# Optimization experiments

Measured on AMD Instinct MI355X. Metric: run time of the kernel, lower is better.

## Reference

```python
import math
import jax, jax.numpy as jnp
import numpy as np

E = 1024
H = 16
D = E // H  # 64

def _l2norm(t, eps=1e-12):
    n = jnp.sqrt(jnp.sum(t * t, axis=-1, keepdims=True))
    return t / jnp.maximum(n, eps)

def setup_inputs() -> dict:
    key = jax.random.key(0)
    ks = jax.random.split(key, 10)
    s = 0.02
    x = jax.random.normal(ks[0], (2, 4096, E), dtype=jnp.float32)
    Wq = jax.random.normal(ks[1], (E, E), dtype=jnp.float32) * s
    Wk = jax.random.normal(ks[2], (E, E), dtype=jnp.float32) * s
    Wv = jax.random.normal(ks[3], (E, E), dtype=jnp.float32) * s
    Walpha = jax.random.normal(ks[4], (E, H), dtype=jnp.float32) * s
    Wbeta = jax.random.normal(ks[5], (E, H), dtype=jnp.float32) * s
    A_log = jnp.linspace(0.0, math.log(16.0), H).astype(jnp.float32)
    dt_bias = jnp.zeros((H,), dtype=jnp.float32)
    Wgate = jax.random.normal(ks[6], (E, E), dtype=jnp.float32) * s
    Wout = jax.random.normal(ks[7], (E, E), dtype=jnp.float32) * s
    rms_w = jnp.ones((D,), dtype=jnp.float32)
    return {"x": x, "Wq": Wq, "Wk": Wk, "Wv": Wv, "Walpha": Walpha,
            "Wbeta": Wbeta, "A_log": A_log, "dt_bias": dt_bias,
            "Wgate": Wgate, "Wout": Wout, "rms_w": rms_w}

def reference(x, Wq, Wk, Wv, Walpha, Wbeta, A_log, dt_bias, Wgate, Wout, rms_w):
    b, s, _ = x.shape
    q = (x @ Wq).reshape(b, s, H, D)
    k = (x @ Wk).reshape(b, s, H, D)
    v = (x @ Wv).reshape(b, s, H, D)
    q = _l2norm(q) / math.sqrt(D)
    k = _l2norm(k)
    # gates: alpha in (0,1], beta in (0,1)   [b,s,H]
    dt = jax.nn.softplus(x @ Walpha + dt_bias)
    alpha = jnp.exp(-jnp.exp(A_log) * dt)
    beta = jax.nn.sigmoid(x @ Wbeta)

    # time-major for scan: [s,b,H,D] / [s,b,H]
    qT = jnp.moveaxis(q, 1, 0)
    kT = jnp.moveaxis(k, 1, 0)
    vT = jnp.moveaxis(v, 1, 0)
    aT = jnp.moveaxis(alpha, 1, 0)
    bT = jnp.moveaxis(beta, 1, 0)

    state0 = jnp.zeros((b, H, D, D), dtype=x.dtype)

    def step(state, inp):
        q_t, k_t, v_t, a_t, b_t = inp  # [b,H,D] x3, [b,H] x2
        state = a_t[..., None, None] * state
        stored = jnp.einsum('bhij,bhj->bhi', state, k_t)
        delta = b_t[..., None] * (v_t - stored)
        state = state + jnp.einsum('bhi,bhj->bhij', delta, k_t)
        o_t = jnp.einsum('bhij,bhj->bhi', state, q_t)
        return state, o_t

    # q,k,v are [s,b,H,D] -> per-step [b,H,D]
    qs = jnp.swapaxes(qT, 1, 2).swapaxes(1, 1)  # keep [s,b,H,D]
    _, outs = jax.lax.scan(step, state0, (qT, kT, vT, aT, bT))
    out = jnp.moveaxis(outs, 0, 1)  # [b,s,H,D]

    # RMSNorm over head_dim
    var = jnp.mean(out * out, axis=-1, keepdims=True)
    out = out * jax.lax.rsqrt(var + 1e-6) * rms_w

    out = out.reshape(b, s, E)
    gate = jax.nn.silu(x @ Wgate)
    return (out * gate) @ Wout
```

## Files before the change

kernel.cpp:

```cpp
#include <hip/hip_runtime.h>
#include <cstdint>
#include <cstddef>

typedef __bf16 bf16;
typedef __bf16 bf16x4 __attribute__((ext_vector_type(4)));
typedef __bf16 bf16x8 __attribute__((ext_vector_type(8)));
typedef float  f32x4  __attribute__((ext_vector_type(4)));

#define GLD_LDS16(gp, lp) \
  __builtin_amdgcn_global_load_lds((__attribute__((address_space(1))) void*)(gp), \
                                   (__attribute__((address_space(3))) void*)(lp), 16, 0, 0)

__device__ __forceinline__ f32x4 f32x4_zero(){ f32x4 v; v[0]=0.f; v[1]=0.f; v[2]=0.f; v[3]=0.f; return v; }

__device__ __forceinline__ f32x4 mfma16x16x32(bf16x8 a, bf16x8 b, f32x4 c){
  return __builtin_amdgcn_mfma_f32_16x16x32_bf16(a, b, c, 0, 0, 0);
}
__device__ __forceinline__ bf16x8 frag64(const bf16* base, int row0, int kk, int lane){
  return *(const bf16x8*)&base[(row0 + (lane&15))*64 + kk*32 + (lane>>4)*8];
}
__device__ __forceinline__ bf16x8 fragSwz(const bf16* base, int row0, int kk, int lane){
  const int row = row0 + (lane&15);
  const int off = (kk*32 + (lane>>4)*8) ^ ((row&7)<<3);
  return *(const bf16x8*)&base[row*64 + off];
}
struct bf2 { bf16 h, l; };
__device__ __forceinline__ bf2 split2(float v){
  bf2 r; r.h = (bf16)v; r.l = (bf16)(v - (float)r.h); return r;
}

__global__ __launch_bounds__(256) void k_cvt_x(const float* __restrict__ x,
                                               bf16* __restrict__ xh, bf16* __restrict__ xl, int n4){
  int i = blockIdx.x*256 + threadIdx.x;
  if (i < n4){
    float4 v = ((const float4*)x)[i];
    bf16x4 h, l;
    bf2 t0 = split2(v.x); h[0]=t0.h; l[0]=t0.l;
    bf2 t1 = split2(v.y); h[1]=t1.h; l[1]=t1.l;
    bf2 t2 = split2(v.z); h[2]=t2.h; l[2]=t2.l;
    bf2 t3 = split2(v.w); h[3]=t3.h; l[3]=t3.l;
    ((bf16x4*)xh)[i] = h;
    ((bf16x4*)xl)[i] = l;
  }
}

__global__ __launch_bounds__(256) void k_transpose_w(const float* __restrict__ W,
                                                     bf16* __restrict__ Wth, bf16* __restrict__ Wtl){
  __shared__ float tile[32][33];
  const int k0 = blockIdx.x*32, n0 = blockIdx.y*32;
  const int r = threadIdx.x >> 3, c4 = (threadIdx.x & 7)*4;
  float4 v = *(const float4*)&W[(size_t)(k0+r)*1024 + n0 + c4];
  tile[r][c4+0]=v.x; tile[r][c4+1]=v.y; tile[r][c4+2]=v.z; tile[r][c4+3]=v.w;
  __syncthreads();
  bf16x4 h, l;
  bf2 t0 = split2(tile[c4+0][r]); h[0]=t0.h; l[0]=t0.l;
  bf2 t1 = split2(tile[c4+1][r]); h[1]=t1.h; l[1]=t1.l;
  bf2 t2 = split2(tile[c4+2][r]); h[2]=t2.h; l[2]=t2.l;
  bf2 t3 = split2(tile[c4+3][r]); h[3]=t3.h; l[3]=t3.l;
  *(bf16x4*)&Wth[(size_t)(n0+r)*1024 + k0 + c4] = h;
  *(bf16x4*)&Wtl[(size_t)(n0+r)*1024 + k0 + c4] = l;
}

__global__ __launch_bounds__(256) void k_transpose_ab(const float* __restrict__ Wa, const float* __restrict__ Wb,
                                                      bf16* __restrict__ WabTh, bf16* __restrict__ WabTl){
  int p = blockIdx.x*256 + threadIdx.x;
  if (p < 32768){
    int o = p >> 10, k = p & 1023;
    float v = (o < 16) ? Wa[k*16 + o] : Wb[k*16 + (o-16)];
    bf2 s = split2(v);
    WabTh[p] = s.h;
    WabTl[p] = s.l;
  }
}

__global__ __launch_bounds__(256) void k_gemm3(const bf16* __restrict__ Ah, const bf16* __restrict__ Al,
                                               const bf16* __restrict__ Bth, const bf16* __restrict__ Btl,
                                               bf16* __restrict__ Cb, float* __restrict__ Cf){
  __shared__ bf16 Ash[128*32], Asl[128*32];
  __shared__ bf16 Bsh[128*32], Bsl[128*32];
  const int tid = threadIdx.x, lane = tid & 63, w = tid >> 6;
  const int wm = w >> 1, wn = w & 1;
  const size_t m0 = (size_t)blockIdx.x * 128;
  const size_t n0 = (size_t)blockIdx.y * 128;
  f32x4 acc[4][4];
  #pragma unroll
  for (int i=0;i<4;++i)
    #pragma unroll
    for (int j=0;j<4;++j) acc[i][j] = f32x4_zero();

  for (int k0 = 0; k0 < 1024; k0 += 32){
    __syncthreads();
    #pragma unroll
    for (int j = 0; j < 2; ++j){
      const int rbase = 32*w + 16*j;
      const int r = rbase + (lane >> 2);
      const int kk = k0 + (lane & 3)*8;
      GLD_LDS16(&Ah [(m0 + r)*1024 + kk], &Ash[rbase*32]);
      GLD_LDS16(&Al [(m0 + r)*1024 + kk], &Asl[rbase*32]);
      GLD_LDS16(&Bth[(n0 + r)*1024 + kk], &Bsh[rbase*32]);
      GLD_LDS16(&Btl[(n0 + r)*1024 + kk], &Bsl[rbase*32]);
    }
    __syncthreads();
    bf16x8 ah[4], al[4], bh[4], bl[4];
    #pragma unroll
    for (int t=0;t<4;++t){
      ah[t] = *(const bf16x8*)&Ash[(64*wm + 16*t + (lane&15))*32 + (lane>>4)*8];
      al[t] = *(const bf16x8*)&Asl[(64*wm + 16*t + (lane&15))*32 + (lane>>4)*8];
      bh[t] = *(const bf16x8*)&Bsh[(64*wn + 16*t + (lane&15))*32 + (lane>>4)*8];
      bl[t] = *(const bf16x8*)&Bsl[(64*wn + 16*t + (lane&15))*32 + (lane>>4)*8];
    }
    #pragma unroll
    for (int i=0;i<4;++i)
      #pragma unroll
      for (int j=0;j<4;++j){
        f32x4 t = acc[i][j];
        t = mfma16x16x32(ah[i], bh[j], t);
        t = mfma16x16x32(ah[i], bl[j], t);
        t = mfma16x16x32(al[i], bh[j], t);
        acc[i][j] = t;
      }
  }
  #pragma unroll
  for (int i=0;i<4;++i)
    #pragma unroll
    for (int j=0;j<4;++j)
      #pragma unroll
      for (int r=0;r<4;++r){
        size_t row = m0 + 64*wm + 16*i + (lane>>4)*4 + r;
        size_t col = n0 + 64*wn + 16*j + (lane&15);
        float v = acc[i][j][r];
        if (Cf) Cf[row*1024 + col] = v;
        else    Cb[row*1024 + col] = (bf16)v;
      }
}

template<int NRM>
__global__ __launch_bounds__(256) void k_gemm1(const bf16* __restrict__ Ah, const bf16* __restrict__ Bth,
                                               bf16* __restrict__ Cb, float* __restrict__ Cf){
  __shared__ bf16 Ash[128*32];
  __shared__ bf16 Bsh[128*32];
  const int tid = threadIdx.x, lane = tid & 63, w = tid >> 6;
  const int wm = w >> 1, wn = w & 1;
  const size_t m0 = (size_t)blockIdx.x * 128;
  const size_t n0 = (size_t)blockIdx.y * 128;
  f32x4 acc[4][4];
  #pragma unroll
  for (int i=0;i<4;++i)
    #pragma unroll
    for (int j=0;j<4;++j) acc[i][j] = f32x4_zero();

  for (int k0 = 0; k0 < 1024; k0 += 32){
    __syncthreads();
    #pragma unroll
    for (int j = 0; j < 2; ++j){
      const int rbase = 32*w + 16*j;
      const int r = rbase + (lane >> 2);
      const int kk = k0 + (lane & 3)*8;
      GLD_LDS16(&Ah [(m0 + r)*1024 + kk], &Ash[rbase*32]);
      GLD_LDS16(&Bth[(n0 + r)*1024 + kk], &Bsh[rbase*32]);
    }
    __syncthreads();
    bf16x8 ah[4], bh[4];
    #pragma unroll
    for (int t=0;t<4;++t){
      ah[t] = *(const bf16x8*)&Ash[(64*wm + 16*t + (lane&15))*32 + (lane>>4)*8];
      bh[t] = *(const bf16x8*)&Bsh[(64*wn + 16*t + (lane&15))*32 + (lane>>4)*8];
    }
    #pragma unroll
    for (int i=0;i<4;++i)
      #pragma unroll
      for (int j=0;j<4;++j)
        acc[i][j] = mfma16x16x32(ah[i], bh[j], acc[i][j]);
  }
  #pragma unroll
  for (int i=0;i<4;++i)
    #pragma unroll
    for (int r=0;r<4;++r){
      float sc = 1.f;
      if (NRM){
        float ss = 0.f;
        #pragma unroll
        for (int j=0;j<4;++j) ss += acc[i][j][r]*acc[i][j][r];
        ss += __shfl_xor(ss, 1); ss += __shfl_xor(ss, 2);
        ss += __shfl_xor(ss, 4); ss += __shfl_xor(ss, 8);
        sc = (NRM==1 ? 0.125f : 1.0f) / fmaxf(sqrtf(ss), 1e-12f);
      }
      #pragma unroll
      for (int j=0;j<4;++j){
        size_t row = m0 + 64*wm + 16*i + (lane>>4)*4 + r;
        size_t col = n0 + 64*wn + 16*j + (lane&15);
        float v = acc[i][j][r]*sc;
        if (Cf) Cf[row*1024 + col] = v;
        else    Cb[row*1024 + col] = (bf16)v;
      }
    }
}

__global__ __launch_bounds__(256) void k_ab_gemm(const bf16* __restrict__ xh, const bf16* __restrict__ xl,
    const bf16* __restrict__ WabTh, const bf16* __restrict__ WabTl,
    const float* __restrict__ A_log, const float* __restrict__ dt_bias,
    float* __restrict__ logA, float* __restrict__ betap){
  __shared__ bf16 Ash[2][2048], Asl[2][2048];
  const int tid = threadIdx.x, lane = tid & 63, w = tid >> 6;
  const int mt = w >> 1, nt = w & 1;
  const size_t m0 = (size_t)blockIdx.x * 32;
  const int srow = tid >> 3;
  const int scol = 8*((tid & 7) ^ (srow & 7));
  const size_t sg = (m0 + srow)*1024 + scol;

  f32x4 acc = f32x4_zero();
  GLD_LDS16(&xh[sg], &Ash[0][w*512]);
  GLD_LDS16(&xl[sg], &Asl[0][w*512]);
  for (int s = 0; s < 16; ++s){
    const int cur = s & 1;
    __syncthreads();
    if (s + 1 < 16){
      const size_t g = sg + (size_t)(s+1)*64;
      GLD_LDS16(&xh[g], &Ash[cur^1][w*512]);
      GLD_LDS16(&xl[g], &Asl[cur^1][w*512]);
    }
    const int k0 = s*64;
    #pragma unroll
    for (int kk = 0; kk < 2; ++kk){
      bf16x8 aH = fragSwz(Ash[cur], 16*mt, kk, lane);
      bf16x8 aL = fragSwz(Asl[cur], 16*mt, kk, lane);
      const size_t bo = (size_t)(16*nt + (lane&15))*1024 + k0 + kk*32 + (lane>>4)*8;
      bf16x8 bH = *(const bf16x8*)&WabTh[bo];
      bf16x8 bL = *(const bf16x8*)&WabTl[bo];
      acc = mfma16x16x32(aH, bH, acc);
      acc = mfma16x16x32(aH, bL, acc);
      acc = mfma16x16x32(aL, bH, acc);
    }
  }
  const int col = lane & 15;
  #pragma unroll
  for (int r = 0; r < 4; ++r){
    const size_t row = m0 + 16*mt + (lane>>4)*4 + r;
    float v = acc[r];
    if (nt == 0){
      float z = v + dt_bias[col];
      float dt = (z > 20.f) ? z : log1pf(expf(z));
      logA[row*16 + col] = -expf(A_log[col]) * dt;
    } else {
      betap[row*16 + col] = 1.f/(1.f + expf(-v));
    }
  }
}

__device__ __forceinline__ void load_split_tile(const float* f32, const bf16* b16,
                                                size_t tokbase, int h,
                                                bf16* Lh, bf16* Ll, int tid, int nthr){
  for (int i = tid; i < 1024; i += nthr){
    int t = i >> 4, c4 = (i & 15)*4;
    const size_t g = (tokbase + t)*1024 + (size_t)h*64 + c4;
    float4 v;
    if (f32) v = *(const float4*)&f32[g];
    else { bf16x4 b = *(const bf16x4*)&b16[g]; v.x=(float)b[0]; v.y=(float)b[1]; v.z=(float)b[2]; v.w=(float)b[3]; }
    bf16x4 hh, ll;
    bf2 s0 = split2(v.x); hh[0]=s0.h; ll[0]=s0.l;
    bf2 s1 = split2(v.y); hh[1]=s1.h; ll[1]=s1.l;
    bf2 s2 = split2(v.z); hh[2]=s2.h; ll[2]=s2.l;
    bf2 s3 = split2(v.w); hh[3]=s3.h; ll[3]=s3.l;
    const int off = c4 ^ ((t&7)<<3);
    *(bf16x4*)&Lh[t*64 + off] = hh;
    *(bf16x4*)&Ll[t*64 + off] = ll;
  }
}

__global__ __launch_bounds__(128, 4) void k_phaseA(const float* __restrict__ kf32, const bf16* __restrict__ kb16,
    const float* __restrict__ vf, const float* __restrict__ logA, const float* __restrict__ betap,
    bf16* __restrict__ Wg, bf16* __restrict__ Dg, float* __restrict__ Pg, bf16* __restrict__ Bg){
  __shared__ bf16  Kh[4096], Kl_[4096];
  __shared__ float Ef[4096];
  bf16* DT  = Kh;
  bf16* WT  = Kl_;
  bf16* KtT = (bf16*)&Ef[2048];
  const int tid = threadIdx.x, lane = tid & 63, wid = tid >> 6;
  const int c = blockIdx.x, h = blockIdx.y, b = blockIdx.z;
  const size_t tokbase = (size_t)b*4096 + (size_t)c*64;
  const size_t cbase = ((size_t)((b*16 + h)*64 + c)) * 4096;

  load_split_tile(kf32, kb16, tokbase, h, Kh, Kl_, tid, 128);
  const float bet = betap[(tokbase + lane)*16 + h];
  if (tid < 64){
    float la = logA[(tokbase + tid)*16 + h];
    #pragma unroll
    for (int dlt = 1; dlt < 64; dlt <<= 1){
      float o = __shfl_up(la, dlt);
      if (lane >= dlt) la += o;
    }
    Ef[tid] = la;
  }
  __syncthreads();

  #pragma unroll
  for (int tt = 0; tt < 2; ++tt){
    const int t0 = 32*wid + 16*tt;
    #pragma unroll
    for (int tu = 0; tu < 4; ++tu){
      f32x4 accm = f32x4_zero();
      #pragma unroll
      for (int kk = 0; kk < 2; ++kk){
        bf16x8 aH = fragSwz(Kh,  t0,    kk, lane);
        bf16x8 aL = fragSwz(Kl_, t0,    kk, lane);
        bf16x8 bH = fragSwz(Kh,  16*tu, kk, lane);
        bf16x8 bL = fragSwz(Kl_, 16*tu, kk, lane);
        accm = mfma16x16x32(aH, bH, accm);
        accm = mfma16x16x32(aH, bL, accm);
        accm = mfma16x16x32(aL, bH, accm);
      }
      #pragma unroll
      for (int r = 0; r < 4; ++r){
        int row = t0 + (lane>>4)*4 + r, col = 16*tu + (lane&15);
        float ev = (col < row) ? accm[r]*__expf(Ef[row] - Ef[col]) : 0.f;
        if (row > 0) Ef[row*64 + col] = ev;
      }
    }
  }
  __syncthreads();

  float d[64];
  {
    if (wid == 0){
      #pragma unroll
      for (int t = 0; t < 64; ++t)
        d[t] = vf[(tokbase + t)*1024 + h*64 + lane];
    } else {
      #pragma unroll
      for (int t = 0; t < 64; ++t){
        int ks = lane ^ ((t&7)<<3);
        d[t] = __expf(Ef[t]) * ((float)Kh[t*64 + ks] + (float)Kl_[t*64 + ks]);
      }
    }
    #pragma unroll
    for (int bi = 0; bi < 4; ++bi){
      #pragma unroll
      for (int tt = 0; tt < 16; ++tt){
        const int t = 16*bi + tt;
        float s = 0.f;
        #pragma unroll
        for (int j = 0; j < 16; ++j)
          if (j < tt) s += Ef[t*64 + 16*bi + j] * d[16*bi + j];
        d[t] = __shfl(bet, t) * (d[t] - s);
      }
      #pragma unroll
      for (int b2 = bi + 1; b2 < 4; ++b2)
        #pragma unroll
        for (int tt = 0; tt < 16; ++tt){
          const int t = 16*b2 + tt;
          float a0=0.f,a1=0.f,a2=0.f,a3=0.f;
          #pragma unroll
          for (int q = 0; q < 4; ++q){
            float4 e = *(const float4*)&Ef[t*64 + 16*bi + q*4];
            a0 += e.x * d[16*bi + q*4 + 0];
            a1 += e.y * d[16*bi + q*4 + 1];
            a2 += e.z * d[16*bi + q*4 + 2];
            a3 += e.w * d[16*bi + q*4 + 3];
          }
          d[t] -= (a0+a1)+(a2+a3);
        }
    }
  }
  __syncthreads();

  {
    const float gsc = __expf(Ef[63] - Ef[lane]);
    for (int i = tid; i < 4096; i += 128){
      int t = lane, j = i >> 6;
      int ks = j ^ ((t&7)<<3);
      float kv = (float)Kh[t*64 + ks] + (float)Kl_[t*64 + ks];
      KtT[j*64 + (t ^ ((j&7)<<3))] = (bf16)(gsc * kv);
    }
  }
  __syncthreads();

  const float gL = __expf(Ef[63]);
  {
    bf16* myT = wid ? WT : DT;
    #pragma unroll
    for (int s4 = 0; s4 < 16; ++s4){
      bf16x4 v4;
      v4[0]=(bf16)d[s4*4+0]; v4[1]=(bf16)d[s4*4+1];
      v4[2]=(bf16)d[s4*4+2]; v4[3]=(bf16)d[s4*4+3];
      *(bf16x4*)&myT[lane*64 + ((s4*4) ^ ((lane&7)<<3))] = v4;
    }
    bf16* myG = wid ? Wg : Dg;
    #pragma unroll
    for (int t = 0; t < 64; ++t)
      myG[cbase + (size_t)t*64 + lane] = (bf16)d[t];
  }
  __syncthreads();

  if (wid == 0){
    #pragma unroll
    for (int tj = 0; tj < 4; ++tj)
      #pragma unroll
      for (int ti = 0; ti < 4; ++ti){
        f32x4 acc = f32x4_zero();
        #pragma unroll
        for (int kk = 0; kk < 2; ++kk)
          acc = mfma16x16x32(fragSwz(KtT, 16*tj, kk, lane), fragSwz(WT, 16*ti, kk, lane), acc);
        #pragma unroll
        for (int r = 0; r < 4; ++r){
          int row = 16*tj + (lane>>4)*4 + r, col = 16*ti + (lane&15);
          Pg[cbase + (size_t)row*64 + col] = ((row == col) ? gL : 0.f) - acc[r];
        }
      }
  } else {
    #pragma unroll
    for (int ti = 0; ti < 4; ++ti)
      #pragma unroll
      for (int tj = 0; tj < 4; ++tj){
        f32x4 acc = f32x4_zero();
        #pragma unroll
        for (int kk = 0; kk < 2; ++kk)
          acc = mfma16x16x32(fragSwz(DT, 16*ti, kk, lane), fragSwz(KtT, 16*tj, kk, lane), acc);
        #pragma unroll
        for (int r = 0; r < 4; ++r){
          int row = 16*ti + (lane>>4)*4 + r, col = 16*tj + (lane&15);
          Bg[cbase + (size_t)row*64 + col] = (bf16)acc[r];
        }
      }
  }
}

__global__ __launch_bounds__(256) void k_phaseB1(const float* __restrict__ Pg, const bf16* __restrict__ Bg,
                                                 float* __restrict__ PsegT, float* __restrict__ BsegF){
  __shared__ bf16 PaccH[4096], PaccL[4096], BaccH[4096], BaccL[4096];
  __shared__ bf16 PcH[4096], PcL[4096];
  __shared__ bf16 BcS[4096];
  const int tid = threadIdx.x, lane = tid & 63, w = tid >> 6;
  const int seg = blockIdx.x;
  const size_t chain = blockIdx.y;
  f32x4 Pr[4], Br[4];
  #pragma unroll
  for (int it = 0; it < 4; ++it){
    #pragma unroll
    for (int r = 0; r < 4; ++r){
      int row = 16*w + (lane>>4)*4 + r, col = 16*it + (lane&15);
      Pr[it][r] = (row == col) ? 1.f : 0.f;
      Br[it][r] = 0.f;
    }
  }
  for (int i = 0; i < 8; ++i){
    const size_t cb = (chain*64 + (size_t)seg*8 + i)*4096;
    #pragma unroll
    for (int it = 0; it < 4; ++it)
      #pragma unroll
      for (int r = 0; r < 4; ++r){
        int row = 16*w + (lane>>4)*4 + r, col = 16*it + (lane&15);
        bf2 sp = split2(Pr[it][r]); PaccH[row*64+col] = sp.h; PaccL[row*64+col] = sp.l;
        bf2 sb = split2(Br[it][r]); BaccH[row*64+col] = sb.h; BaccL[row*64+col] = sb.l;
      }
    __syncthreads();
    for (int j = tid; j < 1024; j += 256){
      float4 pv = ((const float4*)(Pg + cb))[j];
      bf16x4 ph, pl;
      bf2 u0 = split2(pv.x); ph[0]=u0.h; pl[0]=u0.l;
      bf2 u1 = split2(pv.y); ph[1]=u1.h; pl[1]=u1.l;
      bf2 u2 = split2(pv.z); ph[2]=u2.h; pl[2]=u2.l;
      bf2 u3 = split2(pv.w); ph[3]=u3.h; pl[3]=u3.l;
      ((bf16x4*)PcH)[j] = ph; ((bf16x4*)PcL)[j] = pl;
    }
    for (int j = tid; j < 512; j += 256)
      ((uint4*)BcS)[j] = ((const uint4*)(Bg + cb))[j];
    __syncthreads();
    f32x4 nP[4], nB[4];
    #pragma unroll
    for (int it = 0; it < 4; ++it){ nP[it] = f32x4_zero(); nB[it] = f32x4_zero(); }
    #pragma unroll
    for (int kk = 0; kk < 2; ++kk){
      bf16x8 aPH = frag64(PaccH, 16*w, kk, lane), aPL = frag64(PaccL, 16*w, kk, lane);
      bf16x8 aBH = frag64(BaccH, 16*w, kk, lane), aBL = frag64(BaccL, 16*w, kk, lane);
      #pragma unroll
      for (int it = 0; it < 4; ++it){
        bf16x8 bH = frag64(PcH, 16*it, kk, lane), bL = frag64(PcL, 16*it, kk, lane);
        nP[it] = mfma16x16x32(aPH, bH, nP[it]);
        nP[it] = mfma16x16x32(aPH, bL, nP[it]);
        nP[it] = mfma16x16x32(aPL, bH, nP[it]);
        nB[it] = mfma16x16x32(aBH, bH, nB[it]);
        nB[it] = mfma16x16x32(aBH, bL, nB[it]);
        nB[it] = mfma16x16x32(aBL, bH, nB[it]);
      }
    }
    #pragma unroll
    for (int it = 0; it < 4; ++it)
      #pragma unroll
      for (int r = 0; r < 4; ++r){
        int row = 16*w + (lane>>4)*4 + r, col = 16*it + (lane&15);
        Pr[it][r] = nP[it][r];
        Br[it][r] = nB[it][r] + (float)BcS[row*64 + col];
      }
  }
  const size_t sb = (chain*8 + seg)*4096;
  #pragma unroll
  for (int it = 0; it < 4; ++it)
    #pragma unroll
    for (int r = 0; r < 4; ++r){
      int row = 16*w + (lane>>4)*4 + r, col = 16*it + (lane&15);
      PsegT[sb + (size_t)col*64 + row] = Pr[it][r];
      BsegF[sb + (size_t)row*64 + col] = Br[it][r];
    }
}

__global__ __launch_bounds__(256) void k_phaseB2(const float* __restrict__ PsegT, const float* __restrict__ BsegF,
                                                 float* __restrict__ S0g){
  __shared__ bf16 Sh[4096], Sl[4096], Ph[4096], Pl[4096];
  __shared__ float Bf[4096];
  const int tid = threadIdx.x, lane = tid & 63, w = tid >> 6;
  const size_t bid = blockIdx.x;
  f32x4 Sr[4];
  #pragma unroll
  for (int it = 0; it < 4; ++it) Sr[it] = f32x4_zero();
  for (int seg = 0; seg < 8; ++seg){
    const size_t sb  = (bid*8 + seg)*4096;
    const size_t s0b = (bid*64 + (size_t)seg*8)*4096;
    #pragma unroll
    for (int it = 0; it < 4; ++it)
      #pragma unroll
      for (int r = 0; r < 4; ++r){
        int row = 16*w + (lane>>4)*4 + r, col = 16*it + (lane&15);
        S0g[s0b + (size_t)row*64 + col] = Sr[it][r];
        bf2 sp = split2(Sr[it][r]); Sh[row*64+col] = sp.h; Sl[row*64+col] = sp.l;
      }
    __syncthreads();
    for (int j = tid; j < 1024; j += 256){
      float4 pv = ((const float4*)(PsegT + sb))[j];
      bf16x4 ph, pl;
      bf2 u0 = split2(pv.x); ph[0]=u0.h; pl[0]=u0.l;
      bf2 u1 = split2(pv.y); ph[1]=u1.h; pl[1]=u1.l;
      bf2 u2 = split2(pv.z); ph[2]=u2.h; pl[2]=u2.l;
      bf2 u3 = split2(pv.w); ph[3]=u3.h; pl[3]=u3.l;
      ((bf16x4*)Ph)[j] = ph; ((bf16x4*)Pl)[j] = pl;
      ((float4*)Bf)[j] = ((const float4*)(BsegF + sb))[j];
    }
    __syncthreads();
    f32x4 nS[4];
    #pragma unroll
    for (int it = 0; it < 4; ++it) nS[it] = f32x4_zero();
    #pragma unroll
    for (int kk = 0; kk < 2; ++kk){
      bf16x8 aH = frag64(Sh, 16*w, kk, lane), aL = frag64(Sl, 16*w, kk, lane);
      #pragma unroll
      for (int it = 0; it < 4; ++it){
        bf16x8 bH = frag64(Ph, 16*it, kk, lane), bL = frag64(Pl, 16*it, kk, lane);
        nS[it] = mfma16x16x32(aH, bH, nS[it]);
        nS[it] = mfma16x16x32(aH, bL, nS[it]);
        nS[it] = mfma16x16x32(aL, bH, nS[it]);
      }
    }
    #pragma unroll
    for (int it = 0; it < 4; ++it)
      #pragma unroll
      for (int r = 0; r < 4; ++r){
        int row = 16*w + (lane>>4)*4 + r, col = 16*it + (lane&15);
        Sr[it][r] = nS[it][r] + Bf[row*64 + col];
      }
  }
}

__global__ __launch_bounds__(256) void k_phaseB3(const float* __restrict__ Pg, const bf16* __restrict__ Bg,
                                                 float* __restrict__ S0g){
  __shared__ bf16 Sh[4096], Sl[4096], Ph[4096], Pl[4096];
  __shared__ bf16 BcS[4096];
  const int tid = threadIdx.x, lane = tid & 63, w = tid >> 6;
  const int seg = blockIdx.x;
  const size_t chain = blockIdx.y;
  const size_t segbase = chain*64 + (size_t)seg*8;
  f32x4 Sr[4];
  #pragma unroll
  for (int it = 0; it < 4; ++it)
    #pragma unroll
    for (int r = 0; r < 4; ++r){
      int row = 16*w + (lane>>4)*4 + r, col = 16*it + (lane&15);
      Sr[it][r] = S0g[segbase*4096 + (size_t)row*64 + col];
    }
  for (int i = 0; i < 7; ++i){
    const size_t cb = (segbase + i)*4096;
    #pragma unroll
    for (int it = 0; it < 4; ++it)
      #pragma unroll
      for (int r = 0; r < 4; ++r){
        int row = 16*w + (lane>>4)*4 + r, col = 16*it + (lane&15);
        bf2 sp = split2(Sr[it][r]); Sh[row*64+col] = sp.h; Sl[row*64+col] = sp.l;
      }
    __syncthreads();
    for (int j = tid; j < 1024; j += 256){
      float4 pv = ((const float4*)(Pg + cb))[j];
      bf16x4 ph, pl;
      bf2 u0 = split2(pv.x); ph[0]=u0.h; pl[0]=u0.l;
      bf2 u1 = split2(pv.y); ph[1]=u1.h; pl[1]=u1.l;
      bf2 u2 = split2(pv.z); ph[2]=u2.h; pl[2]=u2.l;
      bf2 u3 = split2(pv.w); ph[3]=u3.h; pl[3]=u3.l;
      ((bf16x4*)Ph)[j] = ph; ((bf16x4*)Pl)[j] = pl;
    }
    for (int j = tid; j < 512; j += 256)
      ((uint4*)BcS)[j] = ((const uint4*)(Bg + cb))[j];
    __syncthreads();
    f32x4 nS[4];
    #pragma unroll
    for (int it = 0; it < 4; ++it) nS[it] = f32x4_zero();
    #pragma unroll
    for (int kk = 0; kk < 2; ++kk){
      bf16x8 aH = frag64(Sh, 16*w, kk, lane), aL = frag64(Sl, 16*w, kk, lane);
      #pragma unroll
      for (int it = 0; it < 4; ++it){
        bf16x8 bH = frag64(Ph, 16*it, kk, lane), bL = frag64(Pl, 16*it, kk, lane);
        nS[it] = mfma16x16x32(aH, bH, nS[it]);
        nS[it] = mfma16x16x32(aH, bL, nS[it]);
        nS[it] = mfma16x16x32(aL, bH, nS[it]);
      }
    }
    const size_t outb = (segbase + i + 1)*4096;
    #pragma unroll
    for (int it = 0; it < 4; ++it)
      #pragma unroll
      for (int r = 0; r < 4; ++r){
        int row = 16*w + (lane>>4)*4 + r, col = 16*it + (lane&15);
        float v = nS[it][r] + (float)BcS[row*64 + col];
        Sr[it][r] = v;
        S0g[outb + (size_t)row*64 + col] = v;
      }
  }
}

__global__ __launch_bounds__(256, 2) void k_phaseC(
    const float* __restrict__ qf32, const bf16* __restrict__ qb16,
    const float* __restrict__ kf32, const bf16* __restrict__ kb16,
    const bf16* __restrict__ gf, const float* __restrict__ logA,
    const float* __restrict__ S0g, const bf16* __restrict__ Wg, const bf16* __restrict__ Dg,
    const float* __restrict__ rms_w, bf16* __restrict__ yh, bf16* __restrict__ yl){
  __shared__ bf16 Qh[4096], Ql[4096], Kh[4096], Klo[4096];
  __shared__ bf16 Wl_[4096], Dl_[4096];
  __shared__ bf16 S0h[4096], S0l[4096];
  __shared__ bf16 AAg[4096];
  __shared__ bf16 BDt[4096];
  const int tid = threadIdx.x, lane = tid & 63, w = tid >> 6;
  const int c = blockIdx.x, h = blockIdx.y, b = blockIdx.z;
  const size_t tokbase = (size_t)b*4096 + (size_t)c*64;
  const size_t cbase = ((size_t)((b*16 + h)*64 + c)) * 4096;

  load_split_tile(qf32, qb16, tokbase, h, Qh, Ql, tid, 256);
  load_split_tile(kf32, kb16, tokbase, h, Kh, Klo, tid, 256);
  for (int i = tid; i < 512; i += 256){
    int r = i >> 3, d = r*8 + ((i&7) ^ (r&7));
    ((uint4*)Wl_)[d] = ((const uint4*)(Wg + cbase))[i];
    ((uint4*)Dl_)[d] = ((const uint4*)(Dg + cbase))[i];
  }
  for (int i = tid; i < 1024; i += 256){
    float4 v = ((const float4*)(S0g + cbase))[i];
    bf16x4 sh, sl;
    bf2 t0 = split2(v.x); sh[0]=t0.h; sl[0]=t0.l;
    bf2 t1 = split2(v.y); sh[1]=t1.h; sl[1]=t1.l;
    bf2 t2 = split2(v.z); sh[2]=t2.h; sl[2]=t2.l;
    bf2 t3 = split2(v.w); sh[3]=t3.h; sl[3]=t3.l;
    int t = i >> 4, off = ((i&15)*4) ^ ((t&7)<<3);
    *(bf16x4*)&S0h[t*64 + off] = sh;
    *(bf16x4*)&S0l[t*64 + off] = sl;
  }
  float la = logA[(tokbase + lane)*16 + h];
  #pragma unroll
  for (int dlt = 1; dlt < 64; dlt <<= 1){
    float o = __shfl_up(la, dlt);
    if (lane >= dlt) la += o;
  }
  __syncthreads();

  {
    const int t0 = 16*w;
    #pragma unroll
    for (int tu = 0; tu < 4; ++tu){
      f32x4 accm = f32x4_zero();
      #pragma unroll
      for (int kk = 0; kk < 2; ++kk){
        bf16x8 aH = fragSwz(Qh,  t0,    kk, lane);
        bf16x8 aL = fragSwz(Ql,  t0,    kk, lane);
        bf16x8 bH = fragSwz(Kh,  16*tu, kk, lane);
        bf16x8 bL = fragSwz(Klo, 16*tu, kk, lane);
        accm = mfma16x16x32(aH, bH, accm);
        accm = mfma16x16x32(aH, bL, accm);
        accm = mfma16x16x32(aL, bH, accm);
      }
      #pragma unroll
      for (int r = 0; r < 4; ++r){
        int row = t0 + (lane>>4)*4 + r, col = 16*tu + (lane&15);
        float lgr = __shfl(la, row), lgc = __shfl(la, col);
        float v = (col <= row) ? accm[r]*__expf(lgr - lgc) : 0.f;
        AAg[row*64 + (col ^ ((row&7)<<3))] = (bf16)v;
      }
    }
  }
  {
    const int i0 = 16*w;
    #pragma unroll
    for (int tu = 0; tu < 4; ++tu){
      f32x4 accm = f32x4_zero();
      #pragma unroll
      for (int kk = 0; kk < 2; ++kk){
        bf16x8 aH = fragSwz(S0h, i0,    kk, lane);
        bf16x8 aL = fragSwz(S0l, i0,    kk, lane);
        bf16x8 bb = fragSwz(Wl_, 16*tu, kk, lane);
        accm = mfma16x16x32(aH, bb, accm);
        accm = mfma16x16x32(aL, bb, accm);
      }
      #pragma unroll
      for (int r = 0; r < 4; ++r){
        int row = i0 + (lane>>4)*4 + r, col = 16*tu + (lane&15);
        float v = (float)Dl_[col*64 + (row ^ ((col&7)<<3))] - accm[r];
        BDt[row*64 + (col ^ ((row&7)<<3))] = (bf16)v;
      }
    }
  }
  __syncthreads();
  for (int i = tid; i < 4096; i += 256){
    int t = i >> 6;
    float gq = __expf(__shfl(la, t));
    float v = gq * ((float)Qh[i] + (float)Ql[i]);
    bf2 sp = split2(v);
    Qh[i] = sp.h; Ql[i] = sp.l;
  }
  __syncthreads();
  {
    const int t0 = 16*w;
    f32x4 o_acc[4];
    #pragma unroll
    for (int it = 0; it < 4; ++it) o_acc[it] = f32x4_zero();
    #pragma unroll
    for (int kk = 0; kk < 2; ++kk){
      bf16x8 aQh = fragSwz(Qh, t0, kk, lane);
      bf16x8 aQl = fragSwz(Ql, t0, kk, lane);
      bf16x8 aA  = fragSwz(AAg, t0, kk, lane);
      #pragma unroll
      for (int it = 0; it < 4; ++it){
        bf16x8 bSh = fragSwz(S0h, 16*it, kk, lane);
        bf16x8 bSl = fragSwz(S0l, 16*it, kk, lane);
        bf16x8 bD  = fragSwz(BDt, 16*it, kk, lane);
        f32x4 t = o_acc[it];
        t = mfma16x16x32(aQh, bSh, t);
        t = mfma16x16x32(aQh, bSl, t);
        t = mfma16x16x32(aQl, bSh, t);
        t = mfma16x16x32(aA,  bD,  t);
        o_acc[it] = t;
      }
    }
    float rw[4];
    #pragma unroll
    for (int it = 0; it < 4; ++it) rw[it] = rms_w[16*it + (lane&15)];
    #pragma unroll
    for (int r = 0; r < 4; ++r){
      float ss = 0.f;
      #pragma unroll
      for (int it = 0; it < 4; ++it) ss += o_acc[it][r]*o_acc[it][r];
      ss += __shfl_xor(ss, 1); ss += __shfl_xor(ss, 2);
      ss += __shfl_xor(ss, 4); ss += __shfl_xor(ss, 8);
      const float scale = rsqrtf(ss*(1.f/64.f) + 1e-6f);
      const int row = t0 + (lane>>4)*4 + r;
      const size_t tok = tokbase + row;
      #pragma unroll
      for (int it = 0; it < 4; ++it){
        const int col = 16*it + (lane&15);
        float g = (float)gf[tok*1024 + h*64 + col];
        float sg = g / (1.f + __expf(-g));
        float v = o_acc[it][r]*scale*rw[it]*sg;
        bf2 sp = split2(v);
        yh[tok*1024 + h*64 + col] = sp.h;
        yl[tok*1024 + h*64 + col] = sp.l;
      }
    }
  }
}

extern "C" void kernel_launch(void* const* d_in, const int* in_sizes, int n_in,
                              void* d_out, int out_size, void* d_ws, size_t ws_size,
                              hipStream_t stream){
  const float* x     = (const float*)d_in[0];
  const float* Wq    = (const float*)d_in[1];
  const float* Wk    = (const float*)d_in[2];
  const float* Wv    = (const float*)d_in[3];
  const float* Wa    = (const float*)d_in[4];
  const float* Wb    = (const float*)d_in[5];
  const float* A_log = (const float*)d_in[6];
  const float* dt_b  = (const float*)d_in[7];
  const float* Wgt   = (const float*)d_in[8];
  const float* Wo    = (const float*)d_in[9];
  const float* rms_w = (const float*)d_in[10];

  const bool BIG = ws_size >= (size_t)215000000;

  char* ws = (char*)d_ws;
  size_t off = 0;
  auto alloc = [&](size_t bytes)->char*{
    char* p = ws + off;
    off += (bytes + 255) & ~(size_t)255;
    return p;
  };
  const size_t PLANE = (size_t)8192*1024*2;
  const size_t WPL   = (size_t)1024*1024*2;
  bf16* xh  = (bf16*)alloc(PLANE);
  bf16* xl  = (bf16*)alloc(PLANE);
  bf16* wqh = (bf16*)alloc(WPL); bf16* wql = (bf16*)alloc(WPL);
  bf16* wkh = (bf16*)alloc(WPL); bf16* wkl = (bf16*)alloc(WPL);
  bf16* wvh = (bf16*)alloc(WPL); bf16* wvl = (bf16*)alloc(WPL);
  bf16* wgh = (bf16*)alloc(WPL); bf16* wgl = (bf16*)alloc(WPL);
  bf16* woh = (bf16*)alloc(WPL); bf16* wol = (bf16*)alloc(WPL);
  bf16* WabTh = (bf16*)alloc((size_t)32*1024*2);
  bf16* WabTl = (bf16*)alloc((size_t)32*1024*2);
  float* qf = nullptr; bf16* qb = nullptr;
  float* kf = nullptr; bf16* kb = nullptr;
  if (BIG){ qf = (float*)alloc((size_t)8192*1024*4); kf = (float*)alloc((size_t)8192*1024*4); }
  else    { qb = (bf16*) alloc(PLANE);               kb = (bf16*) alloc(PLANE); }
  float* vf  = (float*)alloc((size_t)8192*1024*4);
  bf16* gfb  = (bf16*)alloc(PLANE);
  float* logA  = (float*)alloc((size_t)8192*16*4);
  float* betap = (float*)alloc((size_t)8192*16*4);
  bf16* Wg  = (bf16*)alloc((size_t)2048*4096*2);
  bf16* Dg  = (bf16*)alloc((size_t)2048*4096*2);
  float* Pg  = (float*)xh;
  float* S0g = vf;
  bf16* Bg   = wqh;
  float* PsegT = (float*)d_out;
  float* BsegF = (float*)d_out + 1048576;
  bf16* yh = xh;
  bf16* yl = xl;

  k_cvt_x<<<8192, 256, 0, stream>>>(x, xh, xl, 2097152);
  k_transpose_w<<<dim3(32,32), 256, 0, stream>>>(Wq,  wqh, wql);
  k_transpose_w<<<dim3(32,32), 256, 0, stream>>>(Wk,  wkh, wkl);
  k_transpose_w<<<dim3(32,32), 256, 0, stream>>>(Wv,  wvh, wvl);
  k_transpose_w<<<dim3(32,32), 256, 0, stream>>>(Wgt, wgh, wgl);
  k_transpose_w<<<dim3(32,32), 256, 0, stream>>>(Wo,  woh, wol);
  k_transpose_ab<<<128, 256, 0, stream>>>(Wa, Wb, WabTh, WabTl);

  if (BIG){
    k_gemm1<1><<<dim3(64,8), 256, 0, stream>>>(xh, wqh, nullptr, qf);
    k_gemm1<2><<<dim3(64,8), 256, 0, stream>>>(xh, wkh, nullptr, kf);
  } else {
    k_gemm1<1><<<dim3(64,8), 256, 0, stream>>>(xh, wqh, qb, nullptr);
    k_gemm1<2><<<dim3(64,8), 256, 0, stream>>>(xh, wkh, kb, nullptr);
  }
  k_gemm1<0><<<dim3(64,8), 256, 0, stream>>>(xh, wvh, nullptr, vf);
  k_gemm1<0><<<dim3(64,8), 256, 0, stream>>>(xh, wgh, gfb, nullptr);

  k_ab_gemm<<<256, 256, 0, stream>>>(xh, xl, WabTh, WabTl, A_log, dt_b, logA, betap);

  k_phaseA<<<dim3(64,16,2), 128, 0, stream>>>(kf, kb, vf, logA, betap, Wg, Dg, Pg, Bg);
  k_phaseB1<<<dim3(8,32), 256, 0, stream>>>(Pg, Bg, PsegT, BsegF);
  k_phaseB2<<<32, 256, 0, stream>>>(PsegT, BsegF, S0g);
  k_phaseB3<<<dim3(8,32), 256, 0, stream>>>(Pg, Bg, S0g);
  k_phaseC<<<dim3(64,16,2), 256, 0, stream>>>(qf, qb, kf, kb, gfb, logA, S0g, Wg, Dg, rms_w, yh, yl);

  k_gemm3<<<dim3(64,8), 256, 0, stream>>>(yh, yl, woh, wol, nullptr, (float*)d_out);
}
```

Before: 513.9 us.

## Emit pre-split bf16 hi/lo Q,K from projection GEMM and load via async LDS

The Q/K projection GEMM now writes the hi/lo bf16 split directly instead of fp32 (or single bf16), so phaseA and phaseC no longer convert and split on load. They fill shared memory with swizzled global_load_lds copies for Q, K, W and D tiles, and zero the low planes when only the hi plane exists. PhaseA also moves the beta scaling into the decay matrix and the RHS, removing it from the triangular solve. This cuts global bytes read for Q/K and per-element conversion work in both chunk kernels. The cost is extra bf16 stores from the GEMM epilogue, plus a small numerical reordering in the beta handling.

After: 513.1 us. About the same (-0.1%).

```diff
diff --git a/kernel.cpp b/kernel.cpp
--- a/kernel.cpp
+++ b/kernel.cpp
@@ -136,7 +136,8 @@
 
 template<int NRM>
 __global__ __launch_bounds__(256) void k_gemm1(const bf16* __restrict__ Ah, const bf16* __restrict__ Bth,
-                                               bf16* __restrict__ Cb, float* __restrict__ Cf){
+                                               bf16* __restrict__ Cb, float* __restrict__ Cf,
+                                               bf16* __restrict__ Cl){
   __shared__ bf16 Ash[128*32];
   __shared__ bf16 Bsh[128*32];
   const int tid = threadIdx.x, lane = tid & 63, w = tid >> 6;
@@ -190,8 +191,9 @@
         size_t row = m0 + 64*wm + 16*i + (lane>>4)*4 + r;
         size_t col = n0 + 64*wn + 16*j + (lane&15);
         float v = acc[i][j][r]*sc;
-        if (Cf) Cf[row*1024 + col] = v;
-        else    Cb[row*1024 + col] = (bf16)v;
+        if (Cl){ bf2 sp = split2(v); Cb[row*1024 + col] = sp.h; Cl[row*1024 + col] = sp.l; }
+        else if (Cf) Cf[row*1024 + col] = v;
+        else         Cb[row*1024 + col] = (bf16)v;
       }
     }
 }
@@ -247,27 +249,7 @@
   }
 }
 
-__device__ __forceinline__ void load_split_tile(const float* f32, const bf16* b16,
-                                                size_t tokbase, int h,
-                                                bf16* Lh, bf16* Ll, int tid, int nthr){
-  for (int i = tid; i < 1024; i += nthr){
-    int t = i >> 4, c4 = (i & 15)*4;
-    const size_t g = (tokbase + t)*1024 + (size_t)h*64 + c4;
-    float4 v;
-    if (f32) v = *(const float4*)&f32[g];
-    else { bf16x4 b = *(const bf16x4*)&b16[g]; v.x=(float)b[0]; v.y=(float)b[1]; v.z=(float)b[2]; v.w=(float)b[3]; }
-    bf16x4 hh, ll;
-    bf2 s0 = split2(v.x); hh[0]=s0.h; ll[0]=s0.l;
-    bf2 s1 = split2(v.y); hh[1]=s1.h; ll[1]=s1.l;
-    bf2 s2 = split2(v.z); hh[2]=s2.h; ll[2]=s2.l;
-    bf2 s3 = split2(v.w); hh[3]=s3.h; ll[3]=s3.l;
-    const int off = c4 ^ ((t&7)<<3);
-    *(bf16x4*)&Lh[t*64 + off] = hh;
-    *(bf16x4*)&Ll[t*64 + off] = ll;
-  }
-}
-
-__global__ __launch_bounds__(128, 4) void k_phaseA(const float* __restrict__ kf32, const bf16* __restrict__ kb16,
+__global__ __launch_bounds__(128, 4) void k_phaseA(const bf16* __restrict__ khp, const bf16* __restrict__ klp,
     const float* __restrict__ vf, const float* __restrict__ logA, const float* __restrict__ betap,
     bf16* __restrict__ Wg, bf16* __restrict__ Dg, float* __restrict__ Pg, bf16* __restrict__ Bg){
   __shared__ bf16  Kh[4096], Kl_[4096];
@@ -280,7 +262,20 @@
   const size_t tokbase = (size_t)b*4096 + (size_t)c*64;
   const size_t cbase = ((size_t)((b*16 + h)*64 + c)) * 4096;
 
-  load_split_tile(kf32, kb16, tokbase, h, Kh, Kl_, tid, 128);
+  {
+    const int chunk = tid & 7, r0 = tid >> 3;
+    #pragma unroll
+    for (int rr = 0; rr < 4; ++rr){
+      const int row = 16*rr + r0;
+      const size_t g = (tokbase + row)*1024 + (size_t)h*64 + 8*(chunk ^ (row & 7));
+      GLD_LDS16(&khp[g], &Kh[(16*rr + 8*wid)*64]);
+      if (klp) GLD_LDS16(&klp[g], &Kl_[(16*rr + 8*wid)*64]);
+    }
+    if (!klp){
+      uint4 z4; z4.x=0; z4.y=0; z4.z=0; z4.w=0;
+      for (int z = tid; z < 512; z += 128) ((uint4*)Kl_)[z] = z4;
+    }
+  }
   const float bet = betap[(tokbase + lane)*16 + h];
   if (tid < 64){
     float la = logA[(tokbase + tid)*16 + h];
@@ -312,7 +307,8 @@
       #pragma unroll
       for (int r = 0; r < 4; ++r){
         int row = t0 + (lane>>4)*4 + r, col = 16*tu + (lane&15);
-        float ev = (col < row) ? accm[r]*__expf(Ef[row] - Ef[col]) : 0.f;
+        float bR = __shfl(bet, row);
+        float ev = (col < row) ? accm[r]*__expf(Ef[row] - Ef[col])*bR : 0.f;
         if (row > 0) Ef[row*64 + col] = ev;
       }
     }
@@ -324,12 +320,12 @@
     if (wid == 0){
       #pragma unroll
       for (int t = 0; t < 64; ++t)
-        d[t] = vf[(tokbase + t)*1024 + h*64 + lane];
+        d[t] = __shfl(bet, t) * vf[(tokbase + t)*1024 + h*64 + lane];
     } else {
       #pragma unroll
       for (int t = 0; t < 64; ++t){
         int ks = lane ^ ((t&7)<<3);
-        d[t] = __expf(Ef[t]) * ((float)Kh[t*64 + ks] + (float)Kl_[t*64 + ks]);
+        d[t] = __shfl(bet, t) * __expf(Ef[t]) * ((float)Kh[t*64 + ks] + (float)Kl_[t*64 + ks]);
       }
     }
     #pragma unroll
@@ -341,7 +337,7 @@
         #pragma unroll
         for (int j = 0; j < 16; ++j)
           if (j < tt) s += Ef[t*64 + 16*bi + j] * d[16*bi + j];
-        d[t] = __shfl(bet, t) * (d[t] - s);
+        d[t] = d[t] - s;
       }
       #pragma unroll
       for (int b2 = bi + 1; b2 < 4; ++b2)
@@ -625,8 +621,8 @@
 }
 
 __global__ __launch_bounds__(256, 2) void k_phaseC(
-    const float* __restrict__ qf32, const bf16* __restrict__ qb16,
-    const float* __restrict__ kf32, const bf16* __restrict__ kb16,
+    const bf16* __restrict__ qhp, const bf16* __restrict__ qlp,
+    const bf16* __restrict__ khp, const bf16* __restrict__ klp,
     const bf16* __restrict__ gf, const float* __restrict__ logA,
     const float* __restrict__ S0g, const bf16* __restrict__ Wg, const bf16* __restrict__ Dg,
     const float* __restrict__ rms_w, bf16* __restrict__ yh, bf16* __restrict__ yl){
@@ -640,12 +636,25 @@
   const size_t tokbase = (size_t)b*4096 + (size_t)c*64;
   const size_t cbase = ((size_t)((b*16 + h)*64 + c)) * 4096;
 
-  load_split_tile(qf32, qb16, tokbase, h, Qh, Ql, tid, 256);
-  load_split_tile(kf32, kb16, tokbase, h, Kh, Klo, tid, 256);
-  for (int i = tid; i < 512; i += 256){
-    int r = i >> 3, d = r*8 + ((i&7) ^ (r&7));
-    ((uint4*)Wl_)[d] = ((const uint4*)(Wg + cbase))[i];
-    ((uint4*)Dl_)[d] = ((const uint4*)(Dg + cbase))[i];
+  {
+    const int chunk = tid & 7, r0 = tid >> 3;
+    #pragma unroll
+    for (int rr = 0; rr < 2; ++rr){
+      const int row = 32*rr + r0;
+      const int dbase = (32*rr + 8*w)*64;
+      const size_t g = (tokbase + row)*1024 + (size_t)h*64 + 8*(chunk ^ (row & 7));
+      GLD_LDS16(&qhp[g], &Qh[dbase]);
+      if (qlp) GLD_LDS16(&qlp[g], &Ql[dbase]);
+      GLD_LDS16(&khp[g], &Kh[dbase]);
+      if (klp) GLD_LDS16(&klp[g], &Klo[dbase]);
+      const size_t gg = cbase + (size_t)row*64 + 8*(chunk ^ (row & 7));
+      GLD_LDS16(&Wg[gg], &Wl_[dbase]);
+      GLD_LDS16(&Dg[gg], &Dl_[dbase]);
+    }
+    if (!qlp){
+      uint4 z4; z4.x=0; z4.y=0; z4.z=0; z4.w=0;
+      for (int z = tid; z < 512; z += 256){ ((uint4*)Ql)[z] = z4; ((uint4*)Klo)[z] = z4; }
+    }
   }
   for (int i = tid; i < 1024; i += 256){
     float4 v = ((const float4*)(S0g + cbase))[i];
@@ -805,10 +814,15 @@
   bf16* woh = (bf16*)alloc(WPL); bf16* wol = (bf16*)alloc(WPL);
   bf16* WabTh = (bf16*)alloc((size_t)32*1024*2);
   bf16* WabTl = (bf16*)alloc((size_t)32*1024*2);
-  float* qf = nullptr; bf16* qb = nullptr;
-  float* kf = nullptr; bf16* kb = nullptr;
-  if (BIG){ qf = (float*)alloc((size_t)8192*1024*4); kf = (float*)alloc((size_t)8192*1024*4); }
-  else    { qb = (bf16*) alloc(PLANE);               kb = (bf16*) alloc(PLANE); }
+  bf16* qh = nullptr; bf16* ql = nullptr;
+  bf16* kh = nullptr; bf16* kl = nullptr;
+  if (BIG){
+    qh = (bf16*)alloc(PLANE); ql = (bf16*)alloc(PLANE);
+    kh = (bf16*)alloc(PLANE); kl = (bf16*)alloc(PLANE);
+  } else {
+    qh = (bf16*)alloc(PLANE);
+    kh = (bf16*)alloc(PLANE);
+  }
   float* vf  = (float*)alloc((size_t)8192*1024*4);
   bf16* gfb  = (bf16*)alloc(PLANE);
   float* logA  = (float*)alloc((size_t)8192*16*4);
@@ -831,23 +845,18 @@
   k_transpose_w<<<dim3(32,32), 256, 0, stream>>>(Wo,  woh, wol);
   k_transpose_ab<<<128, 256, 0, stream>>>(Wa, Wb, WabTh, WabTl);
 
-  if (BIG){
-    k_gemm1<1><<<dim3(64,8), 256, 0, stream>>>(xh, wqh, nullptr, qf);
-    k_gemm1<2><<<dim3(64,8), 256, 0, stream>>>(xh, wkh, nullptr, kf);
-  } else {
-    k_gemm1<1><<<dim3(64,8), 256, 0, stream>>>(xh, wqh, qb, nullptr);
-    k_gemm1<2><<<dim3(64,8), 256, 0, stream>>>(xh, wkh, kb, nullptr);
-  }
-  k_gemm1<0><<<dim3(64,8), 256, 0, stream>>>(xh, wvh, nullptr, vf);
-  k_gemm1<0><<<dim3(64,8), 256, 0, stream>>>(xh, wgh, gfb, nullptr);
+  k_gemm1<1><<<dim3(64,8), 256, 0, stream>>>(xh, wqh, qh, nullptr, ql);
+  k_gemm1<2><<<dim3(64,8), 256, 0, stream>>>(xh, wkh, kh, nullptr, kl);
+  k_gemm1<0><<<dim3(64,8), 256, 0, stream>>>(xh, wvh, nullptr, vf, nullptr);
+  k_gemm1<0><<<dim3(64,8), 256, 0, stream>>>(xh, wgh, gfb, nullptr, nullptr);
 
   k_ab_gemm<<<256, 256, 0, stream>>>(xh, xl, WabTh, WabTl, A_log, dt_b, logA, betap);
 
-  k_phaseA<<<dim3(64,16,2), 128, 0, stream>>>(kf, kb, vf, logA, betap, Wg, Dg, Pg, Bg);
+  k_phaseA<<<dim3(64,16,2), 128, 0, stream>>>(kh, kl, vf, logA, betap, Wg, Dg, Pg, Bg);
   k_phaseB1<<<dim3(8,32), 256, 0, stream>>>(Pg, Bg, PsegT, BsegF);
   k_phaseB2<<<32, 256, 0, stream>>>(PsegT, BsegF, S0g);
   k_phaseB3<<<dim3(8,32), 256, 0, stream>>>(Pg, Bg, S0g);
-  k_phaseC<<<dim3(64,16,2), 256, 0, stream>>>(qf, qb, kf, kb, gfb, logA, S0g, Wg, Dg, rms_w, yh, yl);
+  k_phaseC<<<dim3(64,16,2), 256, 0, stream>>>(qh, ql, kh, kl, gfb, logA, S0g, Wg, Dg, rms_w, yh, yl);
 
   k_gemm3<<<dim3(64,8), 256, 0, stream>>>(yh, yl, woh, wol, nullptr, (float*)d_out);
 }
```
